# Optimization experiments

Hardware: AMD Instinct MI355X
Metric: run time of the kernel (lower is better)

The kernel has to match this reference:

```python
import jax, jax.numpy as jnp
import numpy as np

B, S, H = 4, 2048, 2048
E, K = 4, 2
FF = 4 * H  # standard MLP expert expansion


def setup_inputs() -> dict:
    key = jax.random.key(0)
    ks = jax.random.split(key, 5)
    sc = 0.02
    return {
        "hidden_states": jax.random.normal(ks[0], (B, S, H), jnp.float32),
        "w_gate": jax.random.normal(ks[1], (H, E), jnp.float32) * sc,
        "b_gate": jnp.zeros((E,), jnp.float32),
        "w1": jax.random.normal(ks[2], (E, H, FF), jnp.float32) * sc,
        "b1": jnp.zeros((E, FF), jnp.float32),
        "w2": jax.random.normal(ks[3], (E, FF, H), jnp.float32) * sc,
        "b2": jnp.zeros((E, H), jnp.float32),
    }


def reference(hidden_states, w_gate, b_gate, w1, b1, w2, b2):
    # Router: linear gate -> softmax -> top-k, renormalized gate weights
    logits = jnp.einsum("bsh,he->bse", hidden_states, w_gate) + b_gate
    probs = jax.nn.softmax(logits, axis=-1)                       # [B,S,E]
    top_p, top_i = jax.lax.top_k(probs, K)                        # [B,S,K]
    gate_w = top_p / jnp.sum(top_p, axis=-1, keepdims=True)

    # Switch-style load-balancing aux loss
    route = jax.nn.one_hot(top_i, E, dtype=probs.dtype)           # [B,S,K,E]
    frac_tokens = jnp.mean(jnp.sum(route, axis=2) / K, axis=(0, 1))  # [E]
    mean_prob = jnp.mean(probs, axis=(0, 1))                      # [E]
    aux_loss = E * jnp.sum(frac_tokens * mean_prob)

    # Dispatch/combine: small fixed expert count -> loop over experts,
    # dense FFN on all tokens, mask via gate weight (0 for unrouted tokens).
    out = jnp.zeros_like(hidden_states)
    for e in range(E):
        w_e = jnp.sum(gate_w * (top_i == e), axis=-1)             # [B,S]
        h = jax.nn.gelu(jnp.einsum("bsh,hf->bsf", hidden_states, w1[e]) + b1[e])
        y = jnp.einsum("bsf,fh->bsh", h, w2[e]) + b2[e]
        out = out + w_e[..., None] * y
    return out, aux_loss
```

## Files before the change

### kernel.cpp

```cpp
#include <hip/hip_runtime.h>

typedef unsigned short u16;
typedef __attribute__((ext_vector_type(8))) short bf16x8;
typedef __attribute__((ext_vector_type(4))) float f32x4;

#define TOK  8192
#define HD   2048
#define FFD  8192
#define NEXP 4
#define CAPE 4352

__device__ __forceinline__ u16 f2bf(float f){
  unsigned u = __float_as_uint(f);
  u += 0x7fffu + ((u >> 16) & 1u);
  return (u16)(u >> 16);
}

__device__ __forceinline__ float gelu_tanh(float x){
  float u = 0.7978845608028654f * (x + 0.044715f * x * x * x);
  return 0.5f * x * (1.0f + tanhf(u));
}

__device__ __forceinline__ void gload_lds16(const void* g, void* l){
  __builtin_amdgcn_global_load_lds((const __attribute__((address_space(1))) void*)g,
                                   (__attribute__((address_space(3))) void*)l, 16, 0, 0);
}

__device__ __forceinline__ f32x4 mfma_bf16(bf16x8 a, bf16x8 b, f32x4 c){
  asm("v_mfma_f32_16x16x32_bf16 %0, %1, %2, %0" : "+v"(c) : "v"(a), "v"(b));
  return c;
}

__global__ __launch_bounds__(256) void cvt_to_bf16(const float* __restrict__ in,
                                                   u16* __restrict__ out, int n4){
  int i = blockIdx.x * 256 + threadIdx.x;
  if (i >= n4) return;
  float4 v = ((const float4*)in)[i];
  ushort4 o;
  o.x = f2bf(v.x); o.y = f2bf(v.y); o.z = f2bf(v.z); o.w = f2bf(v.w);
  ((ushort4*)out)[i] = o;
}

__global__ __launch_bounds__(256) void transpose_cvt(const float* __restrict__ in,
                                                     u16* __restrict__ out, int R, int C){
  __shared__ u16 t[64][138];
  in  += (size_t)blockIdx.z * R * C;
  out += (size_t)blockIdx.z * R * C;
  const int tx = threadIdx.x & 63;
  const int w  = threadIdx.x >> 6;
  const size_t r0 = (size_t)blockIdx.y * 128;
  const size_t c0 = (size_t)blockIdx.x * 64;
  #pragma unroll
  for (int i = 0; i < 32; i++){
    const int r = w * 32 + i;
    t[tx][r] = f2bf(in[(r0 + r) * C + c0 + tx]);
  }
  __syncthreads();
  #pragma unroll
  for (int j = 0; j < 16; j++){
    const int c = j * 4 + w;
    ushort2 o;
    o.x = t[c][2 * tx];
    o.y = t[c][2 * tx + 1];
    *(ushort2*)(out + (c0 + c) * (size_t)R + r0 + 2 * tx) = o;
  }
}

__global__ __launch_bounds__(256) void router_kernel(
    const float* __restrict__ X, const float* __restrict__ wg, const float* __restrict__ bg,
    float* __restrict__ probs, int* __restrict__ topi, float* __restrict__ gatew){
  int t = blockIdx.x;
  const float* x = X + (size_t)t * HD;
  float a0 = 0.f, a1 = 0.f, a2 = 0.f, a3 = 0.f;
  for (int h = threadIdx.x; h < HD; h += 256){
    float xv = x[h];
    float4 w = ((const float4*)wg)[h];
    a0 += xv * w.x; a1 += xv * w.y; a2 += xv * w.z; a3 += xv * w.w;
  }
  __shared__ float red[4][256];
  red[0][threadIdx.x] = a0; red[1][threadIdx.x] = a1;
  red[2][threadIdx.x] = a2; red[3][threadIdx.x] = a3;
  __syncthreads();
  for (int s = 128; s > 0; s >>= 1){
    if (threadIdx.x < (unsigned)s){
      #pragma unroll
      for (int e = 0; e < 4; e++) red[e][threadIdx.x] += red[e][threadIdx.x + s];
    }
    __syncthreads();
  }
  if (threadIdx.x == 0){
    float l[4], p[4];
    #pragma unroll
    for (int e = 0; e < 4; e++) l[e] = red[e][0] + bg[e];
    float mx = fmaxf(fmaxf(l[0], l[1]), fmaxf(l[2], l[3]));
    float s = 0.f;
    #pragma unroll
    for (int e = 0; e < 4; e++){ p[e] = expf(l[e] - mx); s += p[e]; }
    #pragma unroll
    for (int e = 0; e < 4; e++){ p[e] /= s; probs[t * 4 + e] = p[e]; }
    int e0 = 0;
    for (int e = 1; e < 4; e++) if (p[e] > p[e0]) e0 = e;
    int e1 = -1;
    for (int e = 0; e < 4; e++){ if (e == e0) continue; if (e1 < 0 || p[e] > p[e1]) e1 = e; }
    float g = p[e0] + p[e1];
    topi[t * 2] = e0; topi[t * 2 + 1] = e1;
    #pragma unroll
    for (int e = 0; e < 4; e++)
      gatew[(size_t)e * TOK + t] = (e == e0) ? p[e0] / g : (e == e1) ? p[e1] / g : 0.f;
  }
}

__global__ __launch_bounds__(256) void build_lists(const int* __restrict__ topi,
                                                   int* __restrict__ cnt,
                                                   int* __restrict__ lists){
  int t = blockIdx.x * 256 + threadIdx.x;
  if (t >= TOK) return;
  #pragma unroll
  for (int k = 0; k < 2; k++){
    int e = topi[t * 2 + k];
    int p = atomicAdd(cnt + e, 1);
    lists[e * TOK + p] = t;
  }
}

__global__ __launch_bounds__(256) void aux_kernel(const float* __restrict__ probs,
                                                  const int* __restrict__ topi,
                                                  float* __restrict__ out_aux){
  __shared__ float sp[4][256];
  __shared__ float sc[4][256];
  float p[4] = {0,0,0,0}, c[4] = {0,0,0,0};
  for (int t = threadIdx.x; t < TOK; t += 256){
    #pragma unroll
    for (int e = 0; e < 4; e++) p[e] += probs[t * 4 + e];
    c[topi[t * 2]]     += 1.f;
    c[topi[t * 2 + 1]] += 1.f;
  }
  #pragma unroll
  for (int e = 0; e < 4; e++){ sp[e][threadIdx.x] = p[e]; sc[e][threadIdx.x] = c[e]; }
  __syncthreads();
  for (int s = 128; s > 0; s >>= 1){
    if (threadIdx.x < (unsigned)s){
      #pragma unroll
      for (int e = 0; e < 4; e++){
        sp[e][threadIdx.x] += sp[e][threadIdx.x + s];
        sc[e][threadIdx.x] += sc[e][threadIdx.x + s];
      }
    }
    __syncthreads();
  }
  if (threadIdx.x == 0){
    float aux = 0.f;
    #pragma unroll
    for (int e = 0; e < 4; e++)
      aux += (sc[e][0] / (float)(TOK * 2)) * (sp[e][0] / (float)TOK);
    *out_aux = 4.f * aux;
  }
}

template<int EPI, int N, int K, int ATOMIC>
__global__ __launch_bounds__(256) void gemm_97(
    const u16* __restrict__ A, const u16* __restrict__ BT,
    const int* __restrict__ lists, const int* __restrict__ cnt,
    const float* __restrict__ bias,
    u16* __restrict__ Hout,
    const float* __restrict__ gate, float* __restrict__ Cout)
{
  __shared__ __align__(16) u16 As[128 * 64];
  __shared__ __align__(16) u16 Bs[128 * 64];
  const int e = blockIdx.z;
  const int Mv = cnt[e];
  const int* rowidx = lists + (size_t)e * TOK;
  BT   += (size_t)e * N * K;
  bias += (size_t)e * N;
  if (EPI == 0) Hout += (size_t)e * CAPE * FFD;
  else        { A    += (size_t)e * CAPE * FFD; gate += (size_t)e * TOK; }

  const int gx = gridDim.x, gy = gridDim.y;
  const int orig = blockIdx.x + gx * blockIdx.y;
  const int xcd = orig & 7, rank = orig >> 3;
  const int bxl = rank / gy, by = rank % gy;
  const int bx = xcd * (gx >> 3) + bxl;
  const int browg = by * 128;
  if (browg >= Mv) return;
  const size_t bcol = (size_t)bx * 128;

  const int tid = threadIdx.x, lane = tid & 63, w = tid >> 6;
  const int wr = w >> 1, wc = w & 1;
  const int l8 = lane >> 3;
  const int csw  = ((lane & 7) ^ l8) * 8;
  const int sw   = (lane & 7) * 8;
  const int h8   = ((lane >> 4) & 3) * 8;
  const int colk0 = h8 ^ sw, colk1 = (32 + h8) ^ sw;
  const int r16 = lane & 15;

  const u16* bsrc[4]; int bch[4];
  #pragma unroll
  for (int j = 0; j < 4; j++){
    int rb = j * 32 + w * 8;
    bch[j] = rb * 128;
    bsrc[j] = BT + (bcol + rb + l8) * (size_t)K + csw;
  }
  const u16* asrc[4]; int ach[4];
  #pragma unroll
  for (int q = 0; q < 4; q++){
    int rb = wr * 64 + q * 16 + wc * 8;
    ach[q] = rb * 128;
    int rl = browg + rb + l8;
    int ar;
    if (EPI == 0){
      if (rl > Mv - 1) rl = Mv - 1;
      ar = rowidx[rl];
    } else {
      ar = rl;
    }
    asrc[q] = A + (size_t)ar * K + csw;
  }

  f32x4 acc[4][4];
  #pragma unroll
  for (int m = 0; m < 4; m++)
    #pragma unroll
    for (int n = 0; n < 4; n++) acc[m][n] = (f32x4){0.f, 0.f, 0.f, 0.f};
  bf16x8 bC[8];

  const int NT = K / 64;
  for (int t = 0; t < NT; ++t){
    const size_t ko = (size_t)t * 64;
    __syncthreads();
    #pragma unroll
    for (int j = 0; j < 4; j++) gload_lds16(bsrc[j] + ko, (char*)Bs + bch[j]);
    #pragma unroll
    for (int q = 0; q < 4; q++) gload_lds16(asrc[q] + ko, (char*)As + ach[q]);
    __syncthreads();

    #pragma unroll
    for (int nf = 0; nf < 4; nf++){
      const u16* bp = Bs + (wc * 64 + nf * 16 + r16) * 64;
      bC[nf * 2]     = *(const bf16x8*)(bp + colk0);
      bC[nf * 2 + 1] = *(const bf16x8*)(bp + colk1);
    }
    #pragma unroll
    for (int m = 0; m < 4; m++){
      const u16* ap = As + (wr * 64 + m * 16 + r16) * 64;
      bf16x8 a0 = *(const bf16x8*)(ap + colk0);
      bf16x8 a1 = *(const bf16x8*)(ap + colk1);
      #pragma unroll
      for (int nf = 0; nf < 4; nf++){
        acc[m][nf] = mfma_bf16(a0, bC[nf * 2],     acc[m][nf]);
        acc[m][nf] = mfma_bf16(a1, bC[nf * 2 + 1], acc[m][nf]);
      }
    }
  }

  const int cl = r16, rg = (lane >> 4) * 4;
  const size_t c0 = bcol + wc * 64;
  float bv[4];
  #pragma unroll
  for (int nf = 0; nf < 4; nf++) bv[nf] = bias[c0 + nf * 16 + cl];
  #pragma unroll
  for (int mf = 0; mf < 4; mf++){
    const int rbase = browg + wr * 64 + mf * 16 + rg;
    if (EPI == 0){
      #pragma unroll
      for (int nf = 0; nf < 4; nf++){
        const size_t col = c0 + nf * 16 + cl;
        #pragma unroll
        for (int j = 0; j < 4; j++)
          Hout[(size_t)(rbase + j) * N + col] = f2bf(gelu_tanh(acc[mf][nf][j] + bv[nf]));
      }
    } else {
      int   tok[4]; float gv[4];
      #pragma unroll
      for (int j = 0; j < 4; j++){
        const bool ok = (rbase + j) < Mv;
        tok[j] = ok ? rowidx[rbase + j] : -1;
        gv[j]  = ok ? gate[tok[j]] : 0.f;
      }
      #pragma unroll
      for (int nf = 0; nf < 4; nf++){
        const size_t col = c0 + nf * 16 + cl;
        #pragma unroll
        for (int j = 0; j < 4; j++){
          if (tok[j] >= 0){
            const size_t idx = (size_t)tok[j] * N + col;
            float y = gv[j] * (acc[mf][nf][j] + bv[nf]);
            if (ATOMIC) atomicAdd(Cout + idx, y);
            else        Cout[idx] += y;
          }
        }
      }
    }
  }
}

extern "C" void kernel_launch(void* const* d_in, const int* in_sizes, int n_in,
                              void* d_out, int out_size, void* d_ws, size_t ws_size,
                              hipStream_t stream){
  (void)in_sizes; (void)n_in;
  const float* X  = (const float*)d_in[0];
  const float* wg = (const float*)d_in[1];
  const float* bg = (const float*)d_in[2];
  const float* w1 = (const float*)d_in[3];
  const float* b1 = (const float*)d_in[4];
  const float* w2 = (const float*)d_in[5];
  const float* b2 = (const float*)d_in[6];
  float* out = (float*)d_out;

  char* ws = (char*)d_ws;
  size_t off = 0;
  auto alloc = [&](size_t b) -> char* {
    char* p = ws + off;
    off = (off + b + 255) & ~(size_t)255;
    return p;
  };
  u16*   Xb    = (u16*)  alloc((size_t)TOK * HD * 2);
  float* probs = (float*)alloc((size_t)TOK * 4 * 4);
  int*   topi  = (int*)  alloc((size_t)TOK * 2 * 4);
  float* gatew = (float*)alloc((size_t)NEXP * TOK * 4);
  int*   cnt   = (int*)  alloc((size_t)NEXP * 4);
  int*   lists = (int*)  alloc((size_t)NEXP * TOK * 4);
  const size_t common = off;

  const size_t w1t_all = (size_t)NEXP * FFD * HD * 2;
  const size_t w2t_all = (size_t)NEXP * HD * FFD * 2;
  const size_t hb_all  = (size_t)NEXP * CAPE * FFD * 2;
  const bool merged = ws_size >= common + w1t_all + w2t_all + hb_all + 1024;

  hipMemsetAsync(cnt, 0, NEXP * sizeof(int), stream);
  hipMemsetAsync(out, 0, (size_t)TOK * HD * sizeof(float), stream);

  cvt_to_bf16<<<(TOK * HD / 4 + 255) / 256, 256, 0, stream>>>(X, Xb, TOK * HD / 4);
  router_kernel<<<TOK, 256, 0, stream>>>(X, wg, bg, probs, topi, gatew);
  build_lists<<<TOK / 256, 256, 0, stream>>>(topi, cnt, lists);
  aux_kernel<<<1, 256, 0, stream>>>(probs, topi, out + (out_size - 1));

  if (merged){
    u16* W1T = (u16*)alloc(w1t_all);
    u16* W2T = (u16*)alloc(w2t_all);
    u16* Hb  = (u16*)alloc(hb_all);
    transpose_cvt<<<dim3(FFD / 64, HD / 128, NEXP), 256, 0, stream>>>(w1, W1T, HD, FFD);
    transpose_cvt<<<dim3(HD / 64, FFD / 128, NEXP), 256, 0, stream>>>(w2, W2T, FFD, HD);
    gemm_97<0, FFD, HD, 0><<<dim3(FFD / 128, CAPE / 128, NEXP), 256, 0, stream>>>(
        Xb, W1T, lists, cnt, b1, Hb, nullptr, nullptr);
    gemm_97<1, HD, FFD, 1><<<dim3(HD / 128, CAPE / 128, NEXP), 256, 0, stream>>>(
        Hb, W2T, lists, cnt, b2, nullptr, gatew, out);
  } else {
    u16* W1T = (u16*)alloc((size_t)FFD * HD * 2);
    u16* W2T = (u16*)alloc((size_t)HD * FFD * 2);
    u16* Hb  = (u16*)alloc((size_t)CAPE * FFD * 2);
    for (int e = 0; e < NEXP; ++e){
      transpose_cvt<<<dim3(FFD / 64, HD / 128, 1), 256, 0, stream>>>(
          w1 + (size_t)e * HD * FFD, W1T, HD, FFD);
      transpose_cvt<<<dim3(HD / 64, FFD / 128, 1), 256, 0, stream>>>(
          w2 + (size_t)e * FFD * HD, W2T, FFD, HD);
      gemm_97<0, FFD, HD, 0><<<dim3(FFD / 128, CAPE / 128, 1), 256, 0, stream>>>(
          Xb, W1T, lists + e * TOK, cnt + e, b1 + (size_t)e * FFD,
          Hb, nullptr, nullptr);
      gemm_97<1, HD, FFD, 0><<<dim3(HD / 128, CAPE / 128, 1), 256, 0, stream>>>(
          Hb, W2T, lists + e * TOK, cnt + e, b2 + (size_t)e * HD,
          nullptr, gatew + (size_t)e * TOK, out);
    }
  }
}
```

Before: 1.677 ms.

## Build expert token lists with ordered ballot compaction and nontemporal H stores

Result: faster. 1.587 ms (-5.3%).

```diff
diff --git a/kernel.cpp b/kernel.cpp
--- a/kernel.cpp
+++ b/kernel.cpp
@@ -110,16 +110,55 @@
   }
 }
 
-__global__ __launch_bounds__(256) void build_lists(const int* __restrict__ topi,
-                                                   int* __restrict__ cnt,
-                                                   int* __restrict__ lists){
-  int t = blockIdx.x * 256 + threadIdx.x;
-  if (t >= TOK) return;
-  #pragma unroll
-  for (int k = 0; k < 2; k++){
-    int e = topi[t * 2 + k];
-    int p = atomicAdd(cnt + e, 1);
-    lists[e * TOK + p] = t;
+__global__ __launch_bounds__(256) void compact_stage(const int* __restrict__ topi,
+                                                     int* __restrict__ stage,
+                                                     int* __restrict__ cnum){
+  const int c = blockIdx.x, tid = threadIdx.x;
+  const int t = c * 256 + tid;
+  const int lane = tid & 63, w = tid >> 6;
+  const int e0 = topi[t * 2], e1 = topi[t * 2 + 1];
+  __shared__ int wcnt[4][4], woff[4][4];
+  int pos[4]; bool sel[4];
+  #pragma unroll
+  for (int e = 0; e < 4; e++){
+    sel[e] = (e0 == e) || (e1 == e);
+    unsigned long long m = __ballot(sel[e]);
+    pos[e] = __popcll(m & ((1ull << lane) - 1ull));
+    if (lane == 0) wcnt[e][w] = __popcll(m);
+  }
+  __syncthreads();
+  if (tid < 4){
+    int s = 0;
+    #pragma unroll
+    for (int ww = 0; ww < 4; ww++){ woff[tid][ww] = s; s += wcnt[tid][ww]; }
+    cnum[tid * 32 + c] = s;
+  }
+  __syncthreads();
+  #pragma unroll
+  for (int e = 0; e < 4; e++)
+    if (sel[e]) stage[(e * 32 + c) * 256 + woff[e][w] + pos[e]] = t;
+}
+
+__global__ __launch_bounds__(64) void scan_chunks(const int* __restrict__ cnum,
+                                                  int* __restrict__ coff,
+                                                  int* __restrict__ cnt){
+  if (threadIdx.x < 4){
+    int e = threadIdx.x, s = 0;
+    for (int c = 0; c < 32; c++){ coff[e * 32 + c] = s; s += cnum[e * 32 + c]; }
+    cnt[e] = s;
+  }
+}
+
+__global__ __launch_bounds__(256) void compact_write(const int* __restrict__ stage,
+                                                     const int* __restrict__ cnum,
+                                                     const int* __restrict__ coff,
+                                                     int* __restrict__ lists){
+  const int c = blockIdx.x, tid = threadIdx.x;
+  #pragma unroll
+  for (int e = 0; e < 4; e++){
+    const int n = cnum[e * 32 + c];
+    if (tid < n)
+      lists[e * TOK + coff[e * 32 + c] + tid] = stage[(e * 32 + c) * 256 + tid];
   }
 }
 
@@ -265,8 +304,10 @@
       for (int nf = 0; nf < 4; nf++){
         const size_t col = c0 + nf * 16 + cl;
         #pragma unroll
-        for (int j = 0; j < 4; j++)
-          Hout[(size_t)(rbase + j) * N + col] = f2bf(gelu_tanh(acc[mf][nf][j] + bv[nf]));
+        for (int j = 0; j < 4; j++){
+          u16 hv = f2bf(gelu_tanh(acc[mf][nf][j] + bv[nf]));
+          __builtin_nontemporal_store(hv, &Hout[(size_t)(rbase + j) * N + col]);
+        }
       }
     } else {
       int   tok[4]; float gv[4];
@@ -319,6 +360,9 @@
   float* gatew = (float*)alloc((size_t)NEXP * TOK * 4);
   int*   cnt   = (int*)  alloc((size_t)NEXP * 4);
   int*   lists = (int*)  alloc((size_t)NEXP * TOK * 4);
+  int*   stage = (int*)  alloc((size_t)NEXP * 32 * 256 * 4);
+  int*   cnum  = (int*)  alloc((size_t)NEXP * 32 * 4);
+  int*   coff  = (int*)  alloc((size_t)NEXP * 32 * 4);
   const size_t common = off;
 
   const size_t w1t_all = (size_t)NEXP * FFD * HD * 2;
@@ -326,12 +370,13 @@
   const size_t hb_all  = (size_t)NEXP * CAPE * FFD * 2;
   const bool merged = ws_size >= common + w1t_all + w2t_all + hb_all + 1024;
 
-  hipMemsetAsync(cnt, 0, NEXP * sizeof(int), stream);
   hipMemsetAsync(out, 0, (size_t)TOK * HD * sizeof(float), stream);
 
   cvt_to_bf16<<<(TOK * HD / 4 + 255) / 256, 256, 0, stream>>>(X, Xb, TOK * HD / 4);
   router_kernel<<<TOK, 256, 0, stream>>>(X, wg, bg, probs, topi, gatew);
-  build_lists<<<TOK / 256, 256, 0, stream>>>(topi, cnt, lists);
+  compact_stage<<<32, 256, 0, stream>>>(topi, stage, cnum);
+  scan_chunks<<<1, 64, 0, stream>>>(cnum, coff, cnt);
+  compact_write<<<32, 256, 0, stream>>>(stage, cnum, coff, lists);
   aux_kernel<<<1, 256, 0, stream>>>(probs, topi, out + (out_size - 1));
 
   if (merged){
```
